# Performance work log

Hardware: AMD Instinct MI355X
Metric: run time of the kernel (lower is better)

The kernel has to match this reference:

```python
import jax, jax.numpy as jnp
import numpy as np

IN_F, OUT_F, GROUP = 4096, 11008, 128

# NF4 codebook (normalized-float-4 levels), matches NF4_LEVELS in the source
NF4_LEVELS = jnp.array([
    -1.0, -0.6961928009986877, -0.5250730514526367, -0.39491748809814453,
    -0.28444138169288635, -0.18477343022823334, -0.09105003625154495, 0.0,
    0.07958029955625534, 0.16093020141124725, 0.24611230194568634,
    0.33791524171829224, 0.44070982933044434, 0.5626170039176941,
    0.7229568362236023, 1.0], dtype=jnp.float32)


def setup_inputs() -> dict:
    key = jax.random.key(0)
    k0, k1, k2, k3 = jax.random.split(key, 4)
    x = jax.random.normal(k0, (32, 1, IN_F), dtype=jnp.float32)
    # one int32 per packed byte; low nibble = even element code, high nibble = odd
    packed = jax.random.randint(k1, (OUT_F * IN_F // 2,), 0, 256, dtype=jnp.int32)
    # per-group absmax scales (positive)
    scales = jax.random.uniform(k2, (OUT_F * IN_F // GROUP,), dtype=jnp.float32) * 0.02 + 1e-4
    bias_param = jax.random.normal(k3, (OUT_F,), dtype=jnp.float32)
    return {"x": x, "packed": packed, "scales": scales, "bias_param": bias_param}


def dequant_nf4(packed, scales):
    # unpack two 4-bit codes per byte; interleave as quantized[0::2]=low, [1::2]=high
    low = packed & 15
    high = (packed >> 4) & 15
    codes = jnp.stack([low, high], axis=-1).reshape(-1)          # [OUT_F*IN_F]
    vals = NF4_LEVELS[codes]                                      # codebook lookup
    w = (vals.reshape(-1, GROUP) * scales[:, None]).reshape(OUT_F, IN_F)
    return w


def reference(x, packed, scales, bias_param):
    W = dequant_nf4(packed, scales)                               # [OUT_F, IN_F]
    # y = x @ W^T + b  (F.linear semantics)
    return jnp.einsum('bsi,oi->bso', x, W) + bias_param
```

## Files before the change

kernel.cpp:

```cpp
#include <hip/hip_runtime.h>
#include <hip/hip_bf16.h>

#define IN_F   4096
#define OUT_F  11008
#define BATCH  32
#define GROUP  128
#define KSPLIT 4
#define KBLK   (IN_F / KSPLIT)
#define NTILE  64
#define GRID_N (OUT_F / NTILE)
#define OUTSZ  (BATCH * OUT_F)

typedef __attribute__((ext_vector_type(8))) short  bf16x8;
typedef __attribute__((ext_vector_type(4))) float  f32x4;
typedef __attribute__((ext_vector_type(4))) int    i32x4;

static __device__ __constant__ float NF4_LEVELS[16] = {
    -1.0f, -0.6961928009986877f, -0.5250730514526367f, -0.39491748809814453f,
    -0.28444138169288635f, -0.18477343022823334f, -0.09105003625154495f, 0.0f,
    0.07958029955625534f, 0.16093020141124725f, 0.24611230194568634f,
    0.33791524171829224f, 0.44070982933044434f, 0.5626170039176941f,
    0.7229568362236023f, 1.0f};

#define WS_SCT_OFF  262144
#define WS_PART_OFF (262144 + 1409024)

__global__ void prelude_kernel(const float* __restrict__ x,
                               const float* __restrict__ scales,
                               unsigned short* __restrict__ frag,
                               float* __restrict__ sct) {
    const int bid = blockIdx.x, tid = threadIdx.x;
    if (bid < 64) {
        int T  = bid * 256 + tid;
        int st = T >> 13;
        int kb = (T >> 6) & 127;
        int l  = T & 63;
        int row = st * 16 + (l & 15);
        int k0  = kb * 32 + (l >> 4) * 8;
        const float* src = x + (size_t)row * IN_F + k0;
        unsigned w[4];
        #pragma unroll
        for (int e = 0; e < 4; ++e) {
            unsigned lo = __builtin_bit_cast(unsigned short, __float2bfloat16(src[2 * e]));
            unsigned hi = __builtin_bit_cast(unsigned short, __float2bfloat16(src[2 * e + 1]));
            w[e] = lo | (hi << 16);
        }
        i32x4 v = { (int)w[0], (int)w[1], (int)w[2], (int)w[3] };
        *reinterpret_cast<i32x4*>(frag + ((size_t)st * 8192 + kb * 64 + l) * 8) = v;
    } else {
        int B2 = bid - 64;
        int gr = B2 / 43;
        int o  = (B2 % 43) * 256 + tid;
        sct[gr * OUT_F + o] = scales[o * 32 + gr];
    }
}

__global__ __launch_bounds__(256) void nf4_gemm_kernel(
        const int* __restrict__ packed,
        const unsigned short* __restrict__ frag,
        const float* __restrict__ sct,
        float* __restrict__ part)
{
    __shared__ unsigned tabu[256];
    __shared__ unsigned ovl[8192];

    const int tid  = threadIdx.x;
    const int wave = tid >> 6;
    const int lane = tid & 63;
    const int col  = lane & 15;
    const int g    = lane >> 4;

    {
        unsigned lo = __builtin_bit_cast(unsigned short, __float2bfloat16(NF4_LEVELS[tid & 15]));
        unsigned hi = __builtin_bit_cast(unsigned short, __float2bfloat16(NF4_LEVELS[(tid >> 4) & 15]));
        tabu[tid] = lo | (hi << 16);
    }

    const int n0 = blockIdx.x * NTILE;
    const int k0 = blockIdx.y * KBLK;
    const int* psrc = packed + (size_t)(n0 + wave * 16) * (IN_F / 2) + (k0 >> 1);

    #pragma unroll
    for (int r = 0; r < 2; ++r) {
        i32x4 sr[16];
        #pragma unroll
        for (int ii = 0; ii < 16; ++ii) {
            int i = r * 16 + ii;
            int rl = i >> 1, half = i & 1;
            sr[ii] = *reinterpret_cast<const i32x4*>(
                psrc + (size_t)rl * (IN_F / 2) + half * 256 + lane * 4);
        }
        #pragma unroll
        for (int ii = 0; ii < 16; ++ii) {
            int i = r * 16 + ii;
            int rl = i >> 1, half = i & 1;
            int row = wave * 16 + rl;
            int j = half * 64 + lane;
            int d = (j & 0x70) | ((j & 3) << 2) | ((j >> 2) & 3);
            unsigned v = ((unsigned)(sr[ii][0] & 255))
                       | ((unsigned)(sr[ii][1] & 255) << 8)
                       | ((unsigned)(sr[ii][2] & 255) << 16)
                       | ((unsigned)(sr[ii][3] & 255) << 24);
            ovl[(row * 128 + d) ^ ((row & 7) << 2)] = v;
        }
    }
    __syncthreads();

    f32x4 acc[4][2];
    #pragma unroll
    for (int st = 0; st < 4; ++st)
        #pragma unroll
        for (int h = 0; h < 2; ++h)
            acc[st][h] = (f32x4){0.f, 0.f, 0.f, 0.f};

    const unsigned short* f0 = frag;
    const unsigned short* f1 = frag + 65536;
    const int kbb = (k0 >> 5) + wave * 8;

    #pragma unroll
    for (int ss = 0; ss < 2; ++ss) {
        i32x4 cd[4];
        #pragma unroll
        for (int st = 0; st < 4; ++st) {
            int row = st * 16 + col;
            int base = (row * 128 + wave * 32 + ss * 16 + g * 4) ^ ((row & 7) << 2);
            cd[st] = *reinterpret_cast<const i32x4*>(&ovl[base]);
        }
        bf16x8 A0[4], A1[4];
        #pragma unroll
        for (int t = 0; t < 4; ++t) {
            int kb = kbb + ss * 4 + t;
            A0[t] = *reinterpret_cast<const bf16x8*>(f0 + ((size_t)kb * 64 + lane) * 8);
            A1[t] = *reinterpret_cast<const bf16x8*>(f1 + ((size_t)kb * 64 + lane) * 8);
        }
        f32x4 ta[4][2];
        #pragma unroll
        for (int st = 0; st < 4; ++st)
            #pragma unroll
            for (int h = 0; h < 2; ++h)
                ta[st][h] = (f32x4){0.f, 0.f, 0.f, 0.f};

        #pragma unroll
        for (int t = 0; t < 4; ++t) {
            #pragma unroll
            for (int st = 0; st < 4; ++st) {
                unsigned code = (unsigned)cd[st][t];
                i32x4 bu;
                bu[0] = (int)tabu[code & 255u];
                bu[1] = (int)tabu[(code >> 8) & 255u];
                bu[2] = (int)tabu[(code >> 16) & 255u];
                bu[3] = (int)tabu[code >> 24];
                bf16x8 bf = __builtin_bit_cast(bf16x8, bu);
                ta[st][0] = __builtin_amdgcn_mfma_f32_16x16x32_bf16(A0[t], bf, ta[st][0], 0, 0, 0);
                ta[st][1] = __builtin_amdgcn_mfma_f32_16x16x32_bf16(A1[t], bf, ta[st][1], 0, 0, 0);
            }
        }
        const int gr = (k0 >> 7) + wave * 2 + ss;
        #pragma unroll
        for (int st = 0; st < 4; ++st) {
            float sc = sct[gr * OUT_F + n0 + st * 16 + col];
            #pragma unroll
            for (int j = 0; j < 4; ++j) {
                acc[st][0][j] = fmaf(sc, ta[st][0][j], acc[st][0][j]);
                acc[st][1][j] = fmaf(sc, ta[st][1][j], acc[st][1][j]);
            }
        }
    }

    __syncthreads();
    float* red = (float*)ovl;
    #pragma unroll
    for (int st = 0; st < 4; ++st)
        #pragma unroll
        for (int h = 0; h < 2; ++h)
            #pragma unroll
            for (int j = 0; j < 4; ++j)
                red[wave * 2048 + ((st * 2 + h) * 4 + j) * 64 + lane] = acc[st][h][j];
    __syncthreads();

    float* po = part + (size_t)blockIdx.y * OUTSZ;
    #pragma unroll
    for (int q = 0; q < 8; ++q) {
        int i = q * 256 + tid;
        float s = red[i] + red[2048 + i] + red[4096 + i] + red[6144 + i];
        int l2 = i & 63;
        int j  = (i >> 6) & 3;
        int h  = (i >> 8) & 1;
        int st = i >> 9;
        int b  = h * 16 + (l2 >> 4) * 4 + j;
        int o  = n0 + st * 16 + (l2 & 15);
        po[(size_t)b * OUT_F + o] = s;
    }
}

__global__ void reduce_kernel(const float* __restrict__ part,
                              const float* __restrict__ bias,
                              float* __restrict__ out) {
    int t = blockIdx.x * 256 + threadIdx.x;
    int o = t % OUT_F;
    out[t] = part[t] + part[OUTSZ + t] + part[2 * OUTSZ + t] + part[3 * OUTSZ + t]
           + bias[o];
}

extern "C" void kernel_launch(void* const* d_in, const int* in_sizes, int n_in,
                              void* d_out, int out_size, void* d_ws, size_t ws_size,
                              hipStream_t stream) {
    const float* x      = (const float*)d_in[0];
    const int*   packed = (const int*)d_in[1];
    const float* scales = (const float*)d_in[2];
    const float* bias   = (const float*)d_in[3];
    float* out = (float*)d_out;

    char* ws = (char*)d_ws;
    unsigned short* frag = (unsigned short*)ws;
    float* sct  = (float*)(ws + WS_SCT_OFF);
    float* part = (float*)(ws + WS_PART_OFF);

    prelude_kernel<<<1440, 256, 0, stream>>>(x, scales, frag, sct);
    nf4_gemm_kernel<<<dim3(GRID_N, KSPLIT), 256, 0, stream>>>(packed, frag, sct, part);
    reduce_kernel<<<OUTSZ / 256, 256, 0, stream>>>(part, bias, out);
}
```

Measured before the change: 32.61 us.

## Pipeline packed-weight staging with MFMA compute and coalesce partial-output stores

The GEMM kernel now stages only the first half of each block's packed weight slice into LDS up front. It loads and writes the second half in chunks interleaved between the two halves of the first stage's MFMA work, and the K work is split across waves differently. It also adds a launch-bounds occupancy hint of 3 blocks per SM and rewrites the final reduction so each wave writes contiguous output columns. The aim is to hide global-load latency behind compute and to coalesce stores, at the cost of more register pressure and an extra barrier per stage.

```diff
diff --git a/kernel.cpp b/kernel.cpp
--- a/kernel.cpp
+++ b/kernel.cpp
@@ -55,14 +55,14 @@
     }
 }
 
-__global__ __launch_bounds__(256) void nf4_gemm_kernel(
+__global__ __launch_bounds__(256, 3) void nf4_gemm_kernel(
         const int* __restrict__ packed,
         const unsigned short* __restrict__ frag,
         const float* __restrict__ sct,
         float* __restrict__ part)
 {
     __shared__ unsigned tabu[256];
-    __shared__ unsigned ovl[8192];
+    __shared__ unsigned lds[8192];
 
     const int tid  = threadIdx.x;
     const int wave = tid >> 6;
@@ -76,99 +76,135 @@
         tabu[tid] = lo | (hi << 16);
     }
 
-    const int n0 = blockIdx.x * NTILE;
-    const int k0 = blockIdx.y * KBLK;
-    const int* psrc = packed + (size_t)(n0 + wave * 16) * (IN_F / 2) + (k0 >> 1);
-
-    #pragma unroll
-    for (int r = 0; r < 2; ++r) {
-        i32x4 sr[16];
-        #pragma unroll
-        for (int ii = 0; ii < 16; ++ii) {
-            int i = r * 16 + ii;
-            int rl = i >> 1, half = i & 1;
-            sr[ii] = *reinterpret_cast<const i32x4*>(
-                psrc + (size_t)rl * (IN_F / 2) + half * 256 + lane * 4);
-        }
-        #pragma unroll
-        for (int ii = 0; ii < 16; ++ii) {
-            int i = r * 16 + ii;
-            int rl = i >> 1, half = i & 1;
-            int row = wave * 16 + rl;
-            int j = half * 64 + lane;
-            int d = (j & 0x70) | ((j & 3) << 2) | ((j >> 2) & 3);
-            unsigned v = ((unsigned)(sr[ii][0] & 255))
-                       | ((unsigned)(sr[ii][1] & 255) << 8)
-                       | ((unsigned)(sr[ii][2] & 255) << 16)
-                       | ((unsigned)(sr[ii][3] & 255) << 24);
-            ovl[(row * 128 + d) ^ ((row & 7) << 2)] = v;
-        }
+    const int n0    = blockIdx.x * NTILE;
+    const int kint0 = blockIdx.y * 512;
+    const int kbB   = blockIdx.y * 32;
+    const int grB   = blockIdx.y * 8;
+    const int dperm = (lane & 0x30) | ((lane & 3) << 2) | ((lane >> 2) & 3);
+
+    #define STAGE8_LOAD(u, r, sr)                                             \
+        _Pragma("unroll")                                                     \
+        for (int ii = 0; ii < 8; ++ii) {                                      \
+            int rl = (r) * 8 + ii;                                            \
+            sr[ii] = *reinterpret_cast<const i32x4*>(                         \
+                packed + (size_t)(n0 + wave * 16 + rl) * (IN_F / 2)           \
+                       + kint0 + (u) * 256 + lane * 4);                       \
+        }
+
+    #define STAGE8_WRITE(u, r, sr)                                            \
+        _Pragma("unroll")                                                     \
+        for (int ii = 0; ii < 8; ++ii) {                                      \
+            int rl  = (r) * 8 + ii;                                           \
+            int row = wave * 16 + rl;                                         \
+            unsigned v = ((unsigned)(sr[ii][0] & 255))                        \
+                       | ((unsigned)(sr[ii][1] & 255) << 8)                   \
+                       | ((unsigned)(sr[ii][2] & 255) << 16)                  \
+                       | ((unsigned)(sr[ii][3] & 255) << 24);                 \
+            lds[(u) * 4096 + ((row * 64 + dperm) ^ ((row & 7) << 2))] = v;    \
+        }
+
+    {
+        i32x4 sr[8];
+        STAGE8_LOAD(0, 0, sr) STAGE8_WRITE(0, 0, sr)
+        STAGE8_LOAD(0, 1, sr) STAGE8_WRITE(0, 1, sr)
     }
     __syncthreads();
 
     f32x4 acc[4][2];
     #pragma unroll
-    for (int st = 0; st < 4; ++st)
-        #pragma unroll
-        for (int h = 0; h < 2; ++h)
-            acc[st][h] = (f32x4){0.f, 0.f, 0.f, 0.f};
+    for (int st = 0; st < 4; ++st) {
+        acc[st][0] = (f32x4){0.f,0.f,0.f,0.f};
+        acc[st][1] = (f32x4){0.f,0.f,0.f,0.f};
+    }
 
     const unsigned short* f0 = frag;
     const unsigned short* f1 = frag + 65536;
-    const int kbb = (k0 >> 5) + wave * 8;
-
-    #pragma unroll
-    for (int ss = 0; ss < 2; ++ss) {
+
+    #pragma unroll
+    for (int u = 0; u < 2; ++u) {
+        i32x4 sr0[8], sr1[8];
+        if (u == 0) { STAGE8_LOAD(1, 0, sr0) }
+
         i32x4 cd[4];
         #pragma unroll
         for (int st = 0; st < 4; ++st) {
-            int row = st * 16 + col;
-            int base = (row * 128 + wave * 32 + ss * 16 + g * 4) ^ ((row & 7) << 2);
-            cd[st] = *reinterpret_cast<const i32x4*>(&ovl[base]);
-        }
-        bf16x8 A0[4], A1[4];
-        #pragma unroll
-        for (int t = 0; t < 4; ++t) {
-            int kb = kbb + ss * 4 + t;
-            A0[t] = *reinterpret_cast<const bf16x8*>(f0 + ((size_t)kb * 64 + lane) * 8);
-            A1[t] = *reinterpret_cast<const bf16x8*>(f1 + ((size_t)kb * 64 + lane) * 8);
-        }
-        f32x4 ta[4][2];
+            int row  = st * 16 + col;
+            int base = u * 4096 + ((row * 64 + wave * 16 + g * 4) ^ ((row & 7) << 2));
+            cd[st] = *reinterpret_cast<const i32x4*>(&lds[base]);
+        }
+        const int gr = grB + u * 4 + wave;
+        float sc[4];
         #pragma unroll
         for (int st = 0; st < 4; ++st)
-            #pragma unroll
-            for (int h = 0; h < 2; ++h)
-                ta[st][h] = (f32x4){0.f, 0.f, 0.f, 0.f};
-
-        #pragma unroll
-        for (int t = 0; t < 4; ++t) {
-            #pragma unroll
-            for (int st = 0; st < 4; ++st) {
-                unsigned code = (unsigned)cd[st][t];
-                i32x4 bu;
-                bu[0] = (int)tabu[code & 255u];
-                bu[1] = (int)tabu[(code >> 8) & 255u];
-                bu[2] = (int)tabu[(code >> 16) & 255u];
-                bu[3] = (int)tabu[code >> 24];
-                bf16x8 bf = __builtin_bit_cast(bf16x8, bu);
-                ta[st][0] = __builtin_amdgcn_mfma_f32_16x16x32_bf16(A0[t], bf, ta[st][0], 0, 0, 0);
-                ta[st][1] = __builtin_amdgcn_mfma_f32_16x16x32_bf16(A1[t], bf, ta[st][1], 0, 0, 0);
+            sc[st] = sct[gr * OUT_F + n0 + st * 16 + col];
+
+        f32x4 t[4][2];
+        #pragma unroll
+        for (int st = 0; st < 4; ++st) {
+            t[st][0] = (f32x4){0.f,0.f,0.f,0.f};
+            t[st][1] = (f32x4){0.f,0.f,0.f,0.f};
+        }
+
+        {
+            bf16x8 A[4];
+            #pragma unroll
+            for (int tt = 0; tt < 4; ++tt) {
+                int kb = kbB + u * 16 + wave * 4 + tt;
+                A[tt] = *reinterpret_cast<const bf16x8*>(f0 + ((size_t)kb * 64 + lane) * 8);
             }
-        }
-        const int gr = (k0 >> 7) + wave * 2 + ss;
-        #pragma unroll
-        for (int st = 0; st < 4; ++st) {
-            float sc = sct[gr * OUT_F + n0 + st * 16 + col];
+            #pragma unroll
+            for (int tt = 0; tt < 4; ++tt)
+                #pragma unroll
+                for (int st = 0; st < 4; ++st) {
+                    unsigned code = (unsigned)cd[st][tt];
+                    i32x4 bu;
+                    bu[0] = (int)tabu[code & 255u];
+                    bu[1] = (int)tabu[(code >> 8) & 255u];
+                    bu[2] = (int)tabu[(code >> 16) & 255u];
+                    bu[3] = (int)tabu[code >> 24];
+                    t[st][0] = __builtin_amdgcn_mfma_f32_16x16x32_bf16(
+                        A[tt], __builtin_bit_cast(bf16x8, bu), t[st][0], 0, 0, 0);
+                }
+        }
+
+        if (u == 0) { STAGE8_WRITE(1, 0, sr0) STAGE8_LOAD(1, 1, sr1) }
+
+        {
+            bf16x8 A[4];
+            #pragma unroll
+            for (int tt = 0; tt < 4; ++tt) {
+                int kb = kbB + u * 16 + wave * 4 + tt;
+                A[tt] = *reinterpret_cast<const bf16x8*>(f1 + ((size_t)kb * 64 + lane) * 8);
+            }
+            #pragma unroll
+            for (int tt = 0; tt < 4; ++tt)
+                #pragma unroll
+                for (int st = 0; st < 4; ++st) {
+                    unsigned code = (unsigned)cd[st][tt];
+                    i32x4 bu;
+                    bu[0] = (int)tabu[code & 255u];
+                    bu[1] = (int)tabu[(code >> 8) & 255u];
+                    bu[2] = (int)tabu[(code >> 16) & 255u];
+                    bu[3] = (int)tabu[code >> 24];
+                    t[st][1] = __builtin_amdgcn_mfma_f32_16x16x32_bf16(
+                        A[tt], __builtin_bit_cast(bf16x8, bu), t[st][1], 0, 0, 0);
+                }
+        }
+
+        if (u == 0) { STAGE8_WRITE(1, 1, sr1) }
+
+        #pragma unroll
+        for (int st = 0; st < 4; ++st)
             #pragma unroll
             for (int j = 0; j < 4; ++j) {
-                acc[st][0][j] = fmaf(sc, ta[st][0][j], acc[st][0][j]);
-                acc[st][1][j] = fmaf(sc, ta[st][1][j], acc[st][1][j]);
+                acc[st][0][j] = fmaf(sc[st], t[st][0][j], acc[st][0][j]);
+                acc[st][1][j] = fmaf(sc[st], t[st][1][j], acc[st][1][j]);
             }
-        }
-    }
-
-    __syncthreads();
-    float* red = (float*)ovl;
+
+        __syncthreads();
+    }
+
+    float* red = (float*)lds;
     #pragma unroll
     for (int st = 0; st < 4; ++st)
         #pragma unroll
@@ -181,15 +217,15 @@
     float* po = part + (size_t)blockIdx.y * OUTSZ;
     #pragma unroll
     for (int q = 0; q < 8; ++q) {
-        int i = q * 256 + tid;
-        float s = red[i] + red[2048 + i] + red[4096 + i] + red[6144 + i];
-        int l2 = i & 63;
-        int j  = (i >> 6) & 3;
-        int h  = (i >> 8) & 1;
-        int st = i >> 9;
-        int b  = h * 16 + (l2 >> 4) * 4 + j;
-        int o  = n0 + st * 16 + (l2 & 15);
-        po[(size_t)b * OUT_F + o] = s;
+        int b   = q * 4 + wave;
+        int st  = lane >> 4;
+        int c   = lane & 15;
+        int h   = b >> 4;
+        int g2  = (b >> 2) & 3;
+        int j   = b & 3;
+        int slot = ((st * 2 + h) * 4 + j) * 64 + g2 * 16 + c;
+        float s = red[slot] + red[2048 + slot] + red[4096 + slot] + red[6144 + slot];
+        po[(size_t)b * OUT_F + n0 + lane] = s;
     }
 }
 
```

Result: faster. 31.14 us (-4.5%).
